# Kernel tuning notes

Measured on AMD Instinct MI355X. Metric: run time of the kernel, lower is better.

Reference implementation:

```python
import jax, jax.numpy as jnp
import numpy as np

N = 10000; E = 60000; D = 3000; H = 512; L = 128; P = 256
NUM_MASK = 3000  # int(0.3 * N)

def prelu(x, a):
    return jnp.where(x >= 0, x, a * x)

def setup_inputs() -> dict:
    key = jax.random.key(0)
    ks = jax.random.split(key, 32)
    def rn(k, shape, scale=0.02):
        return jax.random.normal(k, shape, jnp.float32) * scale
    inp = {
        'x': jax.random.normal(ks[0], (N, D), jnp.float32),
        'edge_index': jax.random.randint(ks[1], (2, E), 0, N),
        'perm': jax.random.permutation(ks[2], N),
        'shuffle': jax.random.permutation(ks[3], N - NUM_MASK),
        's_W1': rn(ks[4], (D, H)), 's_b1': jnp.zeros((H,), jnp.float32), 's_a': jnp.full((1,), 0.25, jnp.float32),
        's_W2': rn(ks[5], (H, L)), 's_b2': jnp.zeros((L,), jnp.float32),
        't_W1': rn(ks[6], (D, H)), 't_b1': jnp.zeros((H,), jnp.float32), 't_a': jnp.full((1,), 0.25, jnp.float32),
        't_W2': rn(ks[7], (H, L)), 't_b2': jnp.zeros((L,), jnp.float32),
        'p_W1': rn(ks[8], (L, P)), 'p_b1': jnp.zeros((P,), jnp.float32), 'p_a': jnp.full((1,), 0.25, jnp.float32),
        'p_W2': rn(ks[9], (P, L)), 'p_b2': jnp.zeros((L,), jnp.float32),
        'tp_W1': rn(ks[10], (L, P)), 'tp_b1': jnp.zeros((P,), jnp.float32), 'tp_a': jnp.full((1,), 0.25, jnp.float32),
        'tp_W2': rn(ks[11], (P, L)), 'tp_b2': jnp.zeros((L,), jnp.float32),
        'dgi_W': rn(ks[12], (L, L), 0.05),
        'pos_token': rn(ks[13], (1, D)), 'neg_token': rn(ks[14], (1, D)),
        'e2d_W': rn(ks[15], (L, L), 0.05),
        'd_W': rn(ks[16], (L, D)), 'd_b': jnp.zeros((D,), jnp.float32),
    }
    return inp

def reference(x, edge_index, perm, shuffle, s_W1, s_b1, s_a, s_W2, s_b2, t_W1, t_b1, t_a, t_W2, t_b2, p_W1, p_b1, p_a, p_W2, p_b2, tp_W1, tp_b1, tp_a, tp_W2, tp_b2, dgi_W, pos_token, neg_token, e2d_W, d_W, d_b):
    n = x.shape[0]
    # GCN normalization with added self loops (PyG gcn_norm, flow source->target)
    loops = jnp.arange(n)
    src = jnp.concatenate([edge_index[0], loops])
    dst = jnp.concatenate([edge_index[1], loops])
    deg = jax.ops.segment_sum(jnp.ones(dst.shape, x.dtype), dst, n)
    dinv = jnp.where(deg > 0, jax.lax.rsqrt(deg), 0.0)
    enorm = (dinv[src] * dinv[dst])[:, None]  # [E+N, 1]

    def gcn(h, W, b):
        h = h @ W  # transform first, then propagate (PyG GCNConv)
        return jax.ops.segment_sum(h[src] * enorm, dst, n) + b

    # feature masking / corruption (bn=False -> Identity; no dropout at eval)
    mask_nodes = perm[:NUM_MASK]
    keep_nodes = perm[NUM_MASK:]
    use_pos = x.at[mask_nodes].add(pos_token[0])
    use_neg = jnp.zeros_like(x).at[keep_nodes].set(x[keep_nodes][shuffle]).at[mask_nodes].add(neg_token[0])

    # student / teacher two-layer GCN encoders (shared PReLU param per encoder)
    rep_pos = prelu(gcn(prelu(gcn(use_pos, s_W1, s_b1), s_a), s_W2, s_b2), s_a)
    rep_neg = prelu(gcn(prelu(gcn(use_neg, t_W1, t_b1), t_a), t_W2, t_b2), t_a)

    def proj(z, W1, b1, a, W2, b2):
        return prelu(z @ W1 + b1, a) @ W2 + b2

    pos_z = proj(rep_pos[mask_nodes], p_W1, p_b1, p_a, p_W2, p_b2)
    neg_z = proj(rep_neg[mask_nodes], tp_W1, tp_b1, tp_a, tp_W2, tp_b2)

    # DGI loss with sigmoid summary of positive embeddings
    s = jax.nn.sigmoid(pos_z.mean(axis=0))  # [L]
    ws = dgi_W @ s
    pos_d = jax.nn.sigmoid(pos_z @ ws)
    neg_d = jax.nn.sigmoid(neg_z @ ws)
    dgi_loss = -jnp.log(pos_d + 1e-15).mean() - jnp.log(1.0 - neg_d + 1e-15).mean()

    # reconstruction: re-mask latent, single-GCN feature decoder (no activation)
    rec = (rep_pos @ e2d_W).at[mask_nodes].set(0.0)
    rec = gcn(rec, d_W, d_b)

    # SCE loss with alpha = 2
    def l2n(v):
        return v / jnp.maximum(jnp.linalg.norm(v, axis=-1, keepdims=True), 1e-12)
    cos = (l2n(x[mask_nodes]) * l2n(rec[mask_nodes])).sum(axis=-1)
    feat_loss = ((1.0 - cos) ** 2).mean()
    return (feat_loss, dgi_loss)
```

## Files before the change

### kernel.cpp

```cpp
#include <hip/hip_runtime.h>

#define NND 10000
#define EE  60000
#define DD  3000
#define HH  512
#define LL  128
#define PP  256
#define NM  3000

#define KP  3072
#define MP  10240
#define NW  1024
#define KTILES (KP/64)

#define BMT 320
#define BNT 128
#define AH_STR 10240
#define AB_STR 20480
#define BH_STR 4096
#define BB_STR 8192

typedef short bf16x8 __attribute__((ext_vector_type(8)));
typedef float f32x4 __attribute__((ext_vector_type(4)));

__device__ __align__(256) char g_ws[(size_t)176 << 20];

__device__ __forceinline__ unsigned short f2b(float f){
    unsigned int x = __float_as_uint(f);
    unsigned int r = x + 0x7FFFu + ((x >> 16) & 1u);
    return (unsigned short)(r >> 16);
}
__device__ __forceinline__ float b2f(unsigned short u){
    return __uint_as_float(((unsigned int)u) << 16);
}
__device__ __forceinline__ float2 bpair(unsigned int u){
    float2 r;
    r.x = __uint_as_float(u << 16);
    r.y = __uint_as_float(u & 0xffff0000u);
    return r;
}
__device__ __forceinline__ unsigned int packb(float a, float b){
    return (unsigned int)f2b(a) | ((unsigned int)f2b(b) << 16);
}

__device__ __forceinline__ void gl_lds16(const void* g, void* l){
    __builtin_amdgcn_global_load_lds(
        (const __attribute__((address_space(1))) unsigned int*)g,
        (__attribute__((address_space(3))) unsigned int*)l, 16, 0, 0);
}


__global__ void init_k(int* degi, int* cursor, float* scal,
                       float* ptW, float* ntW, float* svecraw, int* ecnt){
    int i = blockIdx.x*256 + threadIdx.x;
    if (i < NND){ degi[i]=0; cursor[i]=0; }
    if (i < 80) scal[i]=0.f;
    if (i == 0) ecnt[0]=0;
    if (i < 128) svecraw[i]=0.f;
    if (i < HH){ ptW[i]=0.f; ntW[i]=0.f; }
}

__global__ void build_k(const int* __restrict__ ei,
                        const int* __restrict__ perm, const int* __restrict__ shuf,
                        int* degi, int* flag, int* negsrc){
    int i = blockIdx.x*256 + threadIdx.x;
    if (i < EE) atomicAdd(&degi[ei[EE + i]], 1);
    if (i < NND){
        int p = perm[i];
        if (i < NM){ flag[p] = 1; negsrc[p] = -1; }
        else       { flag[p] = 0; negsrc[p] = perm[NM + shuf[i - NM]]; }
    }
}

__global__ __launch_bounds__(256) void alloc_k(const int* __restrict__ degi,
                                               float* dinv, int* rowptr, int* ecnt){
    __shared__ int sb[256];
    __shared__ int bbase;
    int t = threadIdx.x;
    int i = blockIdx.x*256 + t;
    int v = (i < NND) ? degi[i] : 0;
    sb[t] = v;
    __syncthreads();
    for (int off = 1; off < 256; off <<= 1){
        int x = 0;
        if (t >= off) x = sb[t - off];
        __syncthreads();
        sb[t] += x;
        __syncthreads();
    }
    if (t == 255) bbase = atomicAdd(ecnt, sb[255]);
    __syncthreads();
    if (i < NND){
        rowptr[i] = bbase + sb[t] - v;
        dinv[i] = 1.f/sqrtf((float)(degi[i] + 1));
    }
}

__global__ void fill_k(const int* __restrict__ ei, const int* __restrict__ rowptr,
                       int* cursor, int* adj){
    int i = blockIdx.x*256 + threadIdx.x;
    if (i < EE){
        int d = ei[EE + i];
        int s = ei[i];
        int p = atomicAdd(&cursor[d], 1);
        adj[rowptr[d] + p] = s;
    }
}

__global__ __launch_bounds__(512) void tok_k(const float* __restrict__ posT,
        const float* __restrict__ negT,
        const float* __restrict__ sW1, const float* __restrict__ tW1,
        float* ptW, float* ntW){
    int b = blockIdx.x; int chunk = blockIdx.y; int j = threadIdx.x;
    const float* tok = b ? negT : posT;
    const float* Wm  = b ? tW1  : sW1;
    float acc = 0.f;
    int d0 = chunk * 47, d1 = d0 + 47; if (d1 > DD) d1 = DD;
    for (int d = d0; d < d1; ++d) acc += tok[d] * Wm[(long)d*HH + j];
    atomicAdd(&((b ? ntW : ptW)[j]), acc);
}


__global__ __launch_bounds__(256) void cast_pad_x_k(const float* __restrict__ x,
                                                    unsigned short* __restrict__ xb){
    long idx = (long)blockIdx.x*256 + threadIdx.x;
    if (idx >= (long)MP*(KP/8)) return;
    int row = (int)(idx / (KP/8));
    int g   = (int)(idx % (KP/8));
    unsigned short o[8] = {0,0,0,0,0,0,0,0};
    if (row < NND && g < DD/8){
        const float* src = x + (long)row*DD + g*8;
        float4 a = *(const float4*)(src);
        float4 b = *(const float4*)(src + 4);
        o[0]=f2b(a.x); o[1]=f2b(a.y); o[2]=f2b(a.z); o[3]=f2b(a.w);
        o[4]=f2b(b.x); o[5]=f2b(b.y); o[6]=f2b(b.z); o[7]=f2b(b.w);
    }
    *(uint4*)(xb + (long)row*KP + g*8) = *(const uint4*)o;
}

struct TBatch {
    const float* in[10];
    unsigned short* out[10];
    int R[10], C[10], OS[10];
    int t0[11];
};

__global__ void transbatch_k(TBatch tb){
    __shared__ unsigned short tile[32][33];
    int b = blockIdx.x;
    int d = 0;
    while (d < 9 && b >= tb.t0[d+1]) d++;
    const float* in = tb.in[d];
    unsigned short* out = tb.out[d];
    int R = tb.R[d], C = tb.C[d], OS = tb.OS[d];
    int lt = b - tb.t0[d];
    int Ctiles = (C + 31) >> 5;
    int rt = lt / Ctiles, ct = lt % Ctiles;
    int rb = rt*32, cb = ct*32;
    int tx = threadIdx.x, ty = threadIdx.y;
    for (int i = ty; i < 32; i += 8){
        int r = rb + i, c = cb + tx;
        tile[i][tx] = (r < R && c < C) ? f2b(in[(long)r*C + c]) : (unsigned short)0;
    }
    __syncthreads();
    for (int i = ty; i < 32; i += 8){
        int c = cb + i, r = rb + tx;
        if (c < C && r < OS) out[(long)c*OS + r] = (r < R) ? tile[tx][i] : (unsigned short)0;
    }
}


#define LDA(PB, MT, KS) (*(const bf16x8*)&As[(PB) + (KS)*AH_STR + a_off + (MT)*512])
#define LDB(PB, NT, KS) (*(const bf16x8*)&Bs[(PB) + (KS)*BH_STR + b_off + (NT)*512])

#define STG_A(KT, PDST, P) gl_lds16(asrc[P] + ((KT)<<6), &As[(PDST) + adst[P]])
#define STG_B(KT, PDST, Q) gl_lds16(bsrc[Q] + ((KT)<<6), &Bs[(PDST) + bdst[Q]])

#define GATE7 asm volatile("s_waitcnt vmcnt(7)" ::: "memory")
#define GATE0 asm volatile("s_waitcnt vmcnt(0)" ::: "memory")
#define NOOPS ((void)0)
#define AFENCE asm volatile("" ::: "memory")
#define BARR  { AFENCE; __builtin_amdgcn_s_barrier(); AFENCE; }

#define TILE_BODY(S1_STMT, S2_STMT, GATE_STMT) {                                  \
    bf16x8 af_[5][2], bf_[4][2];                                                  \
    _Pragma("unroll") for (int nt = 0; nt < 4; ++nt){                             \
        bf_[nt][0] = LDB(pB, nt, 0); bf_[nt][1] = LDB(pB, nt, 1); }               \
    _Pragma("unroll") for (int mt = 0; mt < 5; ++mt){                             \
        af_[mt][0] = LDA(pA, mt, 0); af_[mt][1] = LDA(pA, mt, 1); }               \
    S1_STMT;                                                                      \
    __builtin_amdgcn_s_setprio(1);                                                \
    _Pragma("unroll") for (int ks = 0; ks < 2; ++ks)                              \
      _Pragma("unroll") for (int nt = 0; nt < 4; ++nt)                            \
        _Pragma("unroll") for (int mt = 0; mt < 2; ++mt)                          \
          acc[mt][nt] = __builtin_amdgcn_mfma_f32_16x16x32_bf16(af_[mt][ks], bf_[nt][ks], acc[mt][nt], 0,0,0); \
    __builtin_amdgcn_s_setprio(0);                                                \
    BARR;                                                                         \
    S2_STMT;                                                                      \
    __builtin_amdgcn_s_setprio(1);                                                \
    _Pragma("unroll") for (int ks = 0; ks < 2; ++ks)                              \
      _Pragma("unroll") for (int nt = 0; nt < 4; ++nt)                            \
        _Pragma("unroll") for (int mt = 2; mt < 5; ++mt)                          \
          acc[mt][nt] = __builtin_amdgcn_mfma_f32_16x16x32_bf16(af_[mt][ks], bf_[nt][ks], acc[mt][nt], 0,0,0); \
    __builtin_amdgcn_s_setprio(0);                                                \
    GATE_STMT;                                                                    \
    BARR;                                                                         \
}

__global__ __launch_bounds__(512, 2) void gemm320(
    const unsigned short* __restrict__ Ag,
    const unsigned short* __restrict__ Bg,
    unsigned short* __restrict__ C,
    int M, int Cstride)
{
    __shared__ __align__(1024) unsigned short As[3*AB_STR];
    __shared__ __align__(1024) unsigned short Bs[2*BB_STR];

    const int bid = blockIdx.x;
    const int swz = (bid & 7)*32 + (bid >> 3);
    const int m0 = (swz >> 3) * BMT;
    const int n0 = (swz & 7) * BNT;

    const int tid = threadIdx.x;
    const int w   = tid >> 6,  l = tid & 63;
    const int wm  = w >> 1,    wn = w & 1;
    const int l16 = l & 15,    quad = l >> 4;

    const int schunk = (l & 3) ^ (((l >> 5) & 1) << 1);
    const int rq8   = ((quad ^ (((l16 >> 3) & 1) << 1)) << 3);
    const int a_off = ((wm*80 + l16) << 5) + rq8;
    const int b_off = ((wn*64 + l16) << 5) + rq8;

    const unsigned short* asrc[5]; int adst[5];
    #pragma unroll
    for (int p = 0; p < 5; ++p){
        int j = 5*w + p, kh = j/20, g = j - kh*20;
        asrc[p] = Ag + (long)(m0 + g*16 + (l >> 2))*KP + (kh << 5) + (schunk << 3);
        adst[p] = kh*AH_STR + g*512;
    }
    const unsigned short* bsrc[2]; int bdst[2];
    #pragma unroll
    for (int q = 0; q < 2; ++q){
        int j = 2*w + q, kh = j >> 3, g = j & 7;
        bsrc[q] = Bg + (long)(n0 + g*16 + (l >> 2))*KP + (kh << 5) + (schunk << 3);
        bdst[q] = kh*BH_STR + g*512;
    }

    f32x4 acc[5][4];
    #pragma unroll
    for (int i = 0; i < 5; ++i)
        #pragma unroll
        for (int j = 0; j < 4; ++j)
            #pragma unroll
            for (int r = 0; r < 4; ++r) acc[i][j][r] = 0.f;

    #pragma unroll
    for (int p = 0; p < 5; ++p) STG_A(0, 0, p);
    #pragma unroll
    for (int q = 0; q < 2; ++q) STG_B(0, 0, q);
    #pragma unroll
    for (int p = 0; p < 5; ++p) STG_A(1, AB_STR, p);
    #pragma unroll
    for (int q = 0; q < 2; ++q) STG_B(1, BB_STR, q);
    GATE7;
    BARR;

    int ab = 0, bb = 0;
    #pragma unroll 1
    for (int t = 0; t < KTILES-2; ++t){
        const int pA  = ab*AB_STR;
        const int pB  = bb*BB_STR;
        const int ab2 = (ab == 0) ? 2 : ab - 1;
        const int pA2 = ab2*AB_STR;
        TILE_BODY({ STG_A(t+2,pA2,0); STG_A(t+2,pA2,1); STG_A(t+2,pA2,2); STG_A(t+2,pA2,3); },
                  { STG_A(t+2,pA2,4); STG_B(t+2,pB,0); STG_B(t+2,pB,1); },
                  GATE7)
        ab = (ab == 2) ? 0 : ab + 1;
        bb ^= 1;
    }
    {
        const int pA = ab*AB_STR, pB = bb*BB_STR;
        TILE_BODY(NOOPS, NOOPS, GATE0)
        ab = (ab == 2) ? 0 : ab + 1;
        bb ^= 1;
    }
    {
        const int pA = ab*AB_STR, pB = bb*BB_STR;
        TILE_BODY(NOOPS, NOOPS, NOOPS)
    }

    #pragma unroll
    for (int mt = 0; mt < 5; ++mt){
        const int rowb = m0 + wm*80 + mt*16 + quad*4;
        #pragma unroll
        for (int nt = 0; nt < 4; ++nt){
            const int col = n0 + wn*64 + nt*16 + l16;
            #pragma unroll
            for (int r = 0; r < 4; ++r){
                const int row = rowb + r;
                if (row < M) C[(long)row*Cstride + col] = f2b(acc[mt][nt][r]);
            }
        }
    }
}

__device__ __forceinline__ void gemm_bt_body(
    const unsigned short* __restrict__ A,
    const unsigned short* __restrict__ BT,
    void* __restrict__ Cv,
    int M, int Nn, int K, int Cstride,
    const float* __restrict__ bias,
    const float* __restrict__ alpha,
    int epi, const int* __restrict__ ridx, int obf)
{
    __shared__ __align__(16) unsigned short As[64*40];
    __shared__ __align__(16) unsigned short Bs[64*40];
    const int m0 = blockIdx.y*64, n0 = blockIdx.x*64;
    const int t = threadIdx.x;
    const int lrow = t >> 2, lk = (t & 3) * 8;
    const int wave = t >> 6, lane = t & 63;
    const int quad = lane >> 4, l16 = lane & 15;
    f32x4 acc[4];
    #pragma unroll
    for (int i = 0; i < 4; i++)
        for (int j = 0; j < 4; j++) acc[i][j] = 0.f;

    const bool arv = (m0 + lrow) < M;
    const bool brv = (n0 + lrow) < Nn;
    long arow = 0;
    if (arv) arow = ridx ? (long)ridx[m0 + lrow] : (long)(m0 + lrow);
    const long arowbase = arow * K;
    const long browbase = (long)(n0 + lrow) * K;

    for (int k0 = 0; k0 < K; k0 += 32){
        int gk = k0 + lk;
        uint4 av = {0u,0u,0u,0u};
        uint4 bv = {0u,0u,0u,0u};
        if (arv) av = *(const uint4*)(A + arowbase + gk);
        if (brv) bv = *(const uint4*)(BT + browbase + gk);
        *(uint4*)(&As[lrow*40 + lk]) = av;
        *(uint4*)(&Bs[lrow*40 + lk]) = bv;
        __syncthreads();
        bf16x8 af = *(const bf16x8*)(&As[(wave*16 + l16)*40 + quad*8]);
        #pragma unroll
        for (int nt = 0; nt < 4; nt++){
            bf16x8 bfr = *(const bf16x8*)(&Bs[(nt*16 + l16)*40 + quad*8]);
            acc[nt] = __builtin_amdgcn_mfma_f32_16x16x32_bf16(af, bfr, acc[nt], 0, 0, 0);
        }
        __syncthreads();
    }

    const int rowb = m0 + wave*16 + quad*4;
    float aval = (epi == 2) ? alpha[0] : 0.f;
    #pragma unroll
    for (int nt = 0; nt < 4; nt++){
        int col = n0 + nt*16 + l16;
        if (col >= Nn) continue;
        float bvv = epi ? bias[col] : 0.f;
        #pragma unroll
        for (int r = 0; r < 4; r++){
            int row = rowb + r;
            if (row < M){
                float v = acc[nt][r] + bvv;
                if (epi == 2 && v < 0.f) v *= aval;
                if (obf) ((unsigned short*)Cv)[(long)row*Cstride + col] = f2b(v);
                else     ((float*)Cv)[(long)row*Cstride + col] = v;
            }
        }
    }
}

__global__ __launch_bounds__(256) void gemm_bt_ex(
    const unsigned short* __restrict__ A,
    const unsigned short* __restrict__ BT,
    void* __restrict__ Cv,
    int M, int Nn, int K, int Cstride,
    const float* __restrict__ bias,
    const float* __restrict__ alpha,
    int epi, const int* __restrict__ ridx, int obf)
{
    gemm_bt_body(A, BT, Cv, M, Nn, K, Cstride, bias, alpha, epi, ridx, obf);
}

__global__ __launch_bounds__(256) void gemm_bt2(
    const unsigned short* __restrict__ A0, const unsigned short* __restrict__ A1,
    const unsigned short* __restrict__ B0, const unsigned short* __restrict__ B1,
    void* __restrict__ C0, void* __restrict__ C1,
    int M, int Nn, int K, int Cstride,
    const float* __restrict__ bias0, const float* __restrict__ bias1,
    const float* __restrict__ al0, const float* __restrict__ al1,
    int epi, const int* __restrict__ ridx, int obf)
{
    if (blockIdx.z == 0)
        gemm_bt_body(A0, B0, C0, M, Nn, K, Cstride, bias0, al0, epi, ridx, obf);
    else
        gemm_bt_body(A1, B1, C1, M, Nn, K, Cstride, bias1, al1, epi, ridx, obf);
}

__global__ __launch_bounds__(256) void gemm_bt3(
    const unsigned short* __restrict__ repP, const unsigned short* __restrict__ repN,
    const unsigned short* __restrict__ pW1T, const unsigned short* __restrict__ tpW1T,
    const unsigned short* __restrict__ e2dWT,
    unsigned short* __restrict__ posH, unsigned short* __restrict__ negH,
    unsigned short* __restrict__ recPre,
    const float* __restrict__ pb1, const float* __restrict__ tpb1,
    const float* __restrict__ pa, const float* __restrict__ tpa,
    const int* __restrict__ perm)
{
    int z = blockIdx.z;
    if (z == 0){
        if (blockIdx.y < 47)
            gemm_bt_body(repP, pW1T, posH, NM, PP, LL, PP, pb1, pa, 2, perm, 1);
    } else if (z == 1){
        if (blockIdx.y < 47)
            gemm_bt_body(repN, tpW1T, negH, NM, PP, LL, PP, tpb1, tpa, 2, perm, 1);
    } else {
        if (blockIdx.x < 2)
            gemm_bt_body(repP, e2dWT, recPre, NND, LL, LL, LL, nullptr, nullptr, 0, nullptr, 1);
    }
}


__global__ __launch_bounds__(256) void agg1_k(const unsigned short* __restrict__ XW,
    const float* __restrict__ ptW, const float* __restrict__ ntW,
    const int* __restrict__ flag, const int* __restrict__ negsrc,
    const float* __restrict__ dinv, const int* __restrict__ rowptr,
    const int* __restrict__ degi, const int* __restrict__ adj,
    const float* __restrict__ sb1, const float* __restrict__ sav,
    const float* __restrict__ tb1, const float* __restrict__ tav,
    unsigned short* __restrict__ H1p, unsigned short* __restrict__ H1n)
{
    int i = blockIdx.x; int t = threadIdx.x;
    int half = t >> 7;
    int c = (t & 127) * 4;
    float di = dinv[i];
    int rs = rowptr[i], re = rs + degi[i];
    int fi = flag[i];
    float a0, a1, a2, a3;

    if (half == 0){
        float p0 = ptW[c], p1 = ptW[c+1], p2 = ptW[c+2], p3 = ptW[c+3];
        uint2 v = *(const uint2*)(XW + (long)i*1024 + c);
        float2 va = bpair(v.x), vb = bpair(v.y);
        float ffi = fi ? 1.f : 0.f;
        a0 = (va.x + ffi*p0)*di; a1 = (va.y + ffi*p1)*di;
        a2 = (vb.x + ffi*p2)*di; a3 = (vb.y + ffi*p3)*di;
        for (int e = rs; e < re; ++e){
            int s = adj[e]; float ds = dinv[s];
            float ffs = flag[s] ? 1.f : 0.f;
            uint2 w = *(const uint2*)(XW + (long)s*1024 + c);
            float2 wa = bpair(w.x), wb = bpair(w.y);
            a0 += (wa.x + ffs*p0)*ds; a1 += (wa.y + ffs*p1)*ds;
            a2 += (wb.x + ffs*p2)*ds; a3 += (wb.y + ffs*p3)*ds;
        }
        float sa_ = sav[0];
        float v0 = di*a0 + sb1[c];   if (v0 < 0.f) v0 *= sa_;
        float v1 = di*a1 + sb1[c+1]; if (v1 < 0.f) v1 *= sa_;
        float v2 = di*a2 + sb1[c+2]; if (v2 < 0.f) v2 *= sa_;
        float v3 = di*a3 + sb1[c+3]; if (v3 < 0.f) v3 *= sa_;
        uint2 o; o.x = packb(v0, v1); o.y = packb(v2, v3);
        *(uint2*)(H1p + (long)i*512 + c) = o;
    } else {
        float n0 = ntW[c], n1 = ntW[c+1], n2 = ntW[c+2], n3 = ntW[c+3];
        if (fi){ a0 = n0*di; a1 = n1*di; a2 = n2*di; a3 = n3*di; }
        else {
            int nsi = negsrc[i];
            uint2 v = *(const uint2*)(XW + (long)nsi*1024 + 512 + c);
            float2 va = bpair(v.x), vb = bpair(v.y);
            a0 = va.x*di; a1 = va.y*di; a2 = vb.x*di; a3 = vb.y*di;
        }
        for (int e = rs; e < re; ++e){
            int s = adj[e]; float ds = dinv[s];
            if (flag[s]){ a0 += n0*ds; a1 += n1*ds; a2 += n2*ds; a3 += n3*ds; }
            else {
                int ns = negsrc[s];
                uint2 w = *(const uint2*)(XW + (long)ns*1024 + 512 + c);
                float2 wa = bpair(w.x), wb = bpair(w.y);
                a0 += wa.x*ds; a1 += wa.y*ds; a2 += wb.x*ds; a3 += wb.y*ds;
            }
        }
        float ta_ = tav[0];
        float v0 = di*a0 + tb1[c];   if (v0 < 0.f) v0 *= ta_;
        float v1 = di*a1 + tb1[c+1]; if (v1 < 0.f) v1 *= ta_;
        float v2 = di*a2 + tb1[c+2]; if (v2 < 0.f) v2 *= ta_;
        float v3 = di*a3 + tb1[c+3]; if (v3 < 0.f) v3 *= ta_;
        uint2 o; o.x = packb(v0, v1); o.y = packb(v2, v3);
        *(uint2*)(H1n + (long)i*512 + c) = o;
    }
}

__global__ __launch_bounds__(128) void agg128_k(
    const unsigned short* __restrict__ In0, const unsigned short* __restrict__ In1,
    const float* __restrict__ dinv, const int* __restrict__ rowptr,
    const int* __restrict__ degi, const int* __restrict__ adj,
    const float* __restrict__ b20, const float* __restrict__ b21,
    const float* __restrict__ a20, const float* __restrict__ a21,
    unsigned short* __restrict__ Out0, unsigned short* __restrict__ Out1)
{
    int i = blockIdx.x, t = threadIdx.x;
    int h = t >> 6;
    int c = (t & 63) * 2;
    const unsigned short* In = h ? In1 : In0;
    const float* b2 = h ? b21 : b20;
    const float* a2 = h ? a21 : a20;
    unsigned short* Out = h ? Out1 : Out0;
    float di = dinv[i];
    int rs = rowptr[i], re = rs + degi[i];
    float2 sv = bpair(*(const unsigned int*)(In + (long)i*128 + c));
    float acc0 = sv.x * di, acc1 = sv.y * di;
    for (int e = rs; e < re; ++e){
        int s = adj[e]; float ds = dinv[s];
        float2 w = bpair(*(const unsigned int*)(In + (long)s*128 + c));
        acc0 += w.x * ds; acc1 += w.y * ds;
    }
    float a = a2[0];
    float v0 = di*acc0 + b2[c];   if (v0 < 0.f) v0 *= a;
    float v1 = di*acc1 + b2[c+1]; if (v1 < 0.f) v1 *= a;
    *(unsigned int*)(Out + (long)i*128 + c) = packb(v0, v1);
}

__global__ __launch_bounds__(64) void aggrec_k(const unsigned short* __restrict__ recPre,
    const float* __restrict__ dinv, const int* __restrict__ rowptr,
    const int* __restrict__ degi, const int* __restrict__ adj,
    const int* __restrict__ flag, const int* __restrict__ perm,
    unsigned short* __restrict__ recAgg)
{
    int b = blockIdx.x, t = threadIdx.x;
    int c = t * 2;
    int i = perm[b];
    float di = dinv[i];
    int rs = rowptr[i], re = rs + degi[i];
    float acc0 = 0.f, acc1 = 0.f;
    for (int e = rs; e < re; ++e){
        int s = adj[e];
        if (!flag[s]){
            float ds = dinv[s];
            float2 w = bpair(*(const unsigned int*)(recPre + (long)s*128 + c));
            acc0 += w.x * ds; acc1 += w.y * ds;
        }
    }
    *(unsigned int*)(recAgg + (long)b*128 + c) = packb(di*acc0, di*acc1);
}


__global__ __launch_bounds__(128) void meanp_k(const float* __restrict__ posZ,
                                               float* svecraw){
    int j = threadIdx.x;
    int r0 = blockIdx.x*64, r1 = r0 + 64; if (r1 > NM) r1 = NM;
    float s = 0.f;
    for (int r = r0; r < r1; ++r) s += posZ[(long)r*128 + j];
    atomicAdd(&svecraw[j], s);
}

__global__ void ws_k(const float* __restrict__ dgiW, const float* __restrict__ svecraw,
                     float* wsv){
    __shared__ float s[128];
    int i = threadIdx.x;
    s[i] = 1.f/(1.f + expf(-svecraw[i]/(float)NM));
    __syncthreads();
    float a = 0.f;
    for (int j = 0; j < 128; ++j) a += dgiW[i*128 + j] * s[j];
    wsv[i] = a;
}

__global__ __launch_bounds__(256) void dgi_k(const float* __restrict__ posZ,
    const float* __restrict__ negZ, const float* __restrict__ wsv, float* scal){
    __shared__ float sp[4], sn[4];
    int wid = threadIdx.x >> 6, lane = threadIdx.x & 63;
    float w0 = wsv[lane], w1 = wsv[64 + lane];
    float accp = 0.f, accn = 0.f;
    for (int row = blockIdx.x*4 + wid; row < 2*NM; row += gridDim.x*4){
        const float* Z = (row < NM) ? posZ : negZ;
        int r = (row < NM) ? row : row - NM;
        float v = Z[(long)r*128 + lane] * w0 + Z[(long)r*128 + 64 + lane] * w1;
        for (int off = 32; off; off >>= 1) v += __shfl_down(v, off, 64);
        if (lane == 0){
            float d = 1.f/(1.f + expf(-v));
            if (row < NM) accp += logf(d + 1e-15f);
            else          accn += logf(1.f - d + 1e-15f);
        }
    }
    if (lane == 0){ sp[wid] = accp; sn[wid] = accn; }
    __syncthreads();
    if (threadIdx.x == 0){
        atomicAdd(&scal[0], sp[0]+sp[1]+sp[2]+sp[3]);
        atomicAdd(&scal[1], sn[0]+sn[1]+sn[2]+sn[3]);
    }
}


__global__ __launch_bounds__(256) void cos_k(const float* __restrict__ x,
    const unsigned short* __restrict__ recMask, const int* __restrict__ perm,
    float* scal){
    int b = blockIdx.x, t = threadIdx.x;
    long xi = (long)perm[b]*DD;
    long ri = (long)b*DD;
    float dot = 0.f, nx = 0.f, nr = 0.f;
    for (int d0 = t*8; d0 < DD; d0 += 2048){
        float4 xa = *(const float4*)(x + xi + d0);
        float4 xb2 = *(const float4*)(x + xi + d0 + 4);
        uint4 rv = *(const uint4*)(recMask + ri + d0);
        float2 r0 = bpair(rv.x), r1 = bpair(rv.y), r2 = bpair(rv.z), r3 = bpair(rv.w);
        dot += xa.x*r0.x + xa.y*r0.y + xa.z*r1.x + xa.w*r1.y
             + xb2.x*r2.x + xb2.y*r2.y + xb2.z*r3.x + xb2.w*r3.y;
        nx  += xa.x*xa.x + xa.y*xa.y + xa.z*xa.z + xa.w*xa.w
             + xb2.x*xb2.x + xb2.y*xb2.y + xb2.z*xb2.z + xb2.w*xb2.w;
        nr  += r0.x*r0.x + r0.y*r0.y + r1.x*r1.x + r1.y*r1.y
             + r2.x*r2.x + r2.y*r2.y + r3.x*r3.x + r3.y*r3.y;
    }
    for (int off = 32; off; off >>= 1){
        dot += __shfl_down(dot, off, 64);
        nx  += __shfl_down(nx,  off, 64);
        nr  += __shfl_down(nr,  off, 64);
    }
    __shared__ float sd[4], sx[4], sr[4];
    int w = t >> 6, lane = t & 63;
    if (lane == 0){ sd[w] = dot; sx[w] = nx; sr[w] = nr; }
    __syncthreads();
    if (t == 0){
        float Dv = sd[0]+sd[1]+sd[2]+sd[3];
        float Xv = sx[0]+sx[1]+sx[2]+sx[3];
        float Rv = sr[0]+sr[1]+sr[2]+sr[3];
        float c = Dv/(fmaxf(sqrtf(Xv),1e-12f)*fmaxf(sqrtf(Rv),1e-12f));
        float e = 1.f - c;
        atomicAdd(&scal[16 + (b & 63)], e*e);
    }
}

__global__ void fin_k(const float* __restrict__ scal, float* out){
    float fs = 0.f;
    for (int i = 0; i < 64; ++i) fs += scal[16 + i];
    float feat = fs/(float)NM;
    float dgi  = -(scal[0]/(float)NM) - (scal[1]/(float)NM);
    out[0] = feat;
    out[1] = dgi;
}


extern "C" void kernel_launch(void* const* d_in, const int* in_sizes, int n_in,
                              void* d_out, int out_size, void* d_ws, size_t ws_size,
                              hipStream_t stream) {
    (void)in_sizes; (void)n_in; (void)out_size; (void)d_ws; (void)ws_size;
    const float* x  = (const float*)d_in[0];
    const int* ei   = (const int*)d_in[1];
    const int* perm = (const int*)d_in[2];
    const int* shuf = (const int*)d_in[3];
    const float* sW1 = (const float*)d_in[4];
    const float* sb1 = (const float*)d_in[5];
    const float* sa  = (const float*)d_in[6];
    const float* sW2 = (const float*)d_in[7];
    const float* sb2 = (const float*)d_in[8];
    const float* tW1 = (const float*)d_in[9];
    const float* tb1 = (const float*)d_in[10];
    const float* ta  = (const float*)d_in[11];
    const float* tW2 = (const float*)d_in[12];
    const float* tb2 = (const float*)d_in[13];
    const float* pW1 = (const float*)d_in[14];
    const float* pb1 = (const float*)d_in[15];
    const float* pa  = (const float*)d_in[16];
    const float* pW2 = (const float*)d_in[17];
    const float* pb2 = (const float*)d_in[18];
    const float* tpW1 = (const float*)d_in[19];
    const float* tpb1 = (const float*)d_in[20];
    const float* tpa  = (const float*)d_in[21];
    const float* tpW2 = (const float*)d_in[22];
    const float* tpb2 = (const float*)d_in[23];
    const float* dgiW = (const float*)d_in[24];
    const float* posT = (const float*)d_in[25];
    const float* negT = (const float*)d_in[26];
    const float* e2dW = (const float*)d_in[27];
    const float* dW   = (const float*)d_in[28];
    const float* db   = (const float*)d_in[29];
    float* out = (float*)d_out;

    void* wsp = nullptr;
    hipGetSymbolAddress(&wsp, HIP_SYMBOL(g_ws));
    char* base = (char*)wsp;
    size_t off = 0;
    auto alloc = [&](size_t b){ size_t o = off; off = (off + b + 255) & ~(size_t)255; return o; };

    float* dinv    = (float*)(base + alloc(NND*4));
    int* degi      = (int*)  (base + alloc(NND*4));
    int* rowptr    = (int*)  (base + alloc(NND*4));
    int* cursor    = (int*)  (base + alloc(NND*4));
    int* adj       = (int*)  (base + alloc(EE*4));
    int* flag      = (int*)  (base + alloc(NND*4));
    int* negsrc    = (int*)  (base + alloc(NND*4));
    int* ecnt      = (int*)  (base + alloc(16*4));
    float* ptW     = (float*)(base + alloc(HH*4));
    float* ntW     = (float*)(base + alloc(HH*4));
    float* svecraw = (float*)(base + alloc(128*4));
    float* wsv     = (float*)(base + alloc(128*4));
    float* scal    = (float*)(base + alloc(80*4));

    unsigned short* xb    = (unsigned short*)(base + alloc((size_t)MP*KP*2));
    unsigned short* W1T   = (unsigned short*)(base + alloc((size_t)NW*KP*2));
    unsigned short* sW2T  = (unsigned short*)(base + alloc((size_t)LL*HH*2));
    unsigned short* tW2T  = (unsigned short*)(base + alloc((size_t)LL*HH*2));
    unsigned short* pW1T  = (unsigned short*)(base + alloc((size_t)PP*LL*2));
    unsigned short* pW2T  = (unsigned short*)(base + alloc((size_t)LL*PP*2));
    unsigned short* tpW1T = (unsigned short*)(base + alloc((size_t)PP*LL*2));
    unsigned short* tpW2T = (unsigned short*)(base + alloc((size_t)LL*PP*2));
    unsigned short* e2dWT = (unsigned short*)(base + alloc((size_t)LL*LL*2));
    unsigned short* dWT   = (unsigned short*)(base + alloc((size_t)DD*LL*2));

    unsigned short* XW      = (unsigned short*)(base + alloc((size_t)NND*1024*2));
    unsigned short* H1p     = (unsigned short*)(base + alloc((size_t)NND*512*2));
    unsigned short* H1n     = (unsigned short*)(base + alloc((size_t)NND*512*2));
    unsigned short* M2p     = (unsigned short*)(base + alloc((size_t)NND*128*2));
    unsigned short* M2n     = (unsigned short*)(base + alloc((size_t)NND*128*2));
    unsigned short* repP    = (unsigned short*)(base + alloc((size_t)NND*128*2));
    unsigned short* repN    = (unsigned short*)(base + alloc((size_t)NND*128*2));
    unsigned short* posH    = (unsigned short*)(base + alloc((size_t)NM*256*2));
    unsigned short* negH    = (unsigned short*)(base + alloc((size_t)NM*256*2));
    float* posZ             = (float*)(base + alloc((size_t)NM*128*4));
    float* negZ             = (float*)(base + alloc((size_t)NM*128*4));
    unsigned short* recPre  = (unsigned short*)(base + alloc((size_t)NND*128*2));
    unsigned short* recAgg  = (unsigned short*)(base + alloc((size_t)NM*128*2));
    unsigned short* recMask = (unsigned short*)(base + alloc((size_t)NM*DD*2));

    init_k<<<(NND+255)/256, 256, 0, stream>>>(degi, cursor, scal, ptW, ntW, svecraw, ecnt);
    build_k<<<(EE+255)/256, 256, 0, stream>>>(ei, perm, shuf, degi, flag, negsrc);
    alloc_k<<<(NND+255)/256, 256, 0, stream>>>(degi, dinv, rowptr, ecnt);
    fill_k<<<(EE+255)/256, 256, 0, stream>>>(ei, rowptr, cursor, adj);
    tok_k<<<dim3(2,64), 512, 0, stream>>>(posT, negT, sW1, tW1, ptW, ntW);

    cast_pad_x_k<<<(int)(((long)MP*(KP/8) + 255)/256), 256, 0, stream>>>(x, xb);
    {
        TBatch tb;
        const float* ins[10] = {sW1, tW1, sW2, tW2, pW1, pW2, tpW1, tpW2, e2dW, dW};
        unsigned short* outs[10] = {W1T, W1T + (size_t)HH*KP, sW2T, tW2T, pW1T, pW2T,
                                    tpW1T, tpW2T, e2dWT, dWT};
        int Rs[10]  = {DD, DD, HH, HH, LL, PP, LL, PP, LL, LL};
        int Cs[10]  = {HH, HH, LL, LL, PP, LL, PP, LL, LL, DD};
        int OSs[10] = {KP, KP, HH, HH, LL, PP, LL, PP, LL, LL};
        int cum = 0;
        for (int d = 0; d < 10; d++){
            tb.in[d] = ins[d]; tb.out[d] = outs[d];
            tb.R[d] = Rs[d]; tb.C[d] = Cs[d]; tb.OS[d] = OSs[d];
            tb.t0[d] = cum;
            cum += (OSs[d]/32) * ((Cs[d] + 31)/32);
        }
        tb.t0[10] = cum;
        transbatch_k<<<cum, dim3(32,8), 0, stream>>>(tb);
    }

    gemm320<<<256, 512, 0, stream>>>(xb, W1T, XW, NND, 1024);
    agg1_k<<<NND, 256, 0, stream>>>(XW, ptW, ntW, flag, negsrc, dinv, rowptr, degi, adj,
                                    sb1, sa, tb1, ta, H1p, H1n);

    gemm_bt2<<<dim3(2,157,2), 256, 0, stream>>>(H1p, H1n, sW2T, tW2T, M2p, M2n,
                                                NND, LL, HH, LL,
                                                nullptr, nullptr, nullptr, nullptr,
                                                0, nullptr, 1);
    agg128_k<<<NND, 128, 0, stream>>>(M2p, M2n, dinv, rowptr, degi, adj,
                                      sb2, tb2, sa, ta, repP, repN);

    gemm_bt3<<<dim3(4,157,3), 256, 0, stream>>>(repP, repN, pW1T, tpW1T, e2dWT,
                                                posH, negH, recPre,
                                                pb1, tpb1, pa, tpa, perm);
    gemm_bt2<<<dim3(2,47,2), 256, 0, stream>>>(posH, negH, pW2T, tpW2T, posZ, negZ,
                                               NM, LL, PP, LL,
                                               pb2, tpb2, nullptr, nullptr, 1, nullptr, 0);

    aggrec_k<<<NM, 64, 0, stream>>>(recPre, dinv, rowptr, degi, adj, flag, perm, recAgg);
    gemm_bt_ex<<<dim3(47,47), 256, 0, stream>>>(recAgg, dWT, recMask, NM, DD, LL, DD,
                                                db, nullptr, 1, nullptr, 1);

    meanp_k<<<47, 128, 0, stream>>>(posZ, svecraw);
    ws_k<<<1, 128, 0, stream>>>(dgiW, svecraw, wsv);
    dgi_k<<<128, 256, 0, stream>>>(posZ, negZ, wsv, scal);

    cos_k<<<NM, 256, 0, stream>>>(x, recMask, perm, scal);

    fin_k<<<1, 1, 0, stream>>>(scal, out);
}
```

Measured before the change: 497.0 us.

## Merge staging kernels, fuse posZ column mean into GEMM, widen small-GEMM K step

Folds the x cast/pad, the weight transposes and the token-times-W1 products into a single staging launch, which removes two kernel launches. The pos-projection GEMM now accumulates column sums in its epilogue through shared memory and atomics. That replaces the separate mean kernel, and the bias is added back inside ws_k. The generic small GEMM also loads 64-wide K slices per barrier instead of 32, halving the number of synchronisations at the cost of more shared memory.

```diff
diff --git a/kernel.cpp b/kernel.cpp
--- a/kernel.cpp
+++ b/kernel.cpp
@@ -107,36 +107,6 @@
     }
 }
 
-__global__ __launch_bounds__(512) void tok_k(const float* __restrict__ posT,
-        const float* __restrict__ negT,
-        const float* __restrict__ sW1, const float* __restrict__ tW1,
-        float* ptW, float* ntW){
-    int b = blockIdx.x; int chunk = blockIdx.y; int j = threadIdx.x;
-    const float* tok = b ? negT : posT;
-    const float* Wm  = b ? tW1  : sW1;
-    float acc = 0.f;
-    int d0 = chunk * 47, d1 = d0 + 47; if (d1 > DD) d1 = DD;
-    for (int d = d0; d < d1; ++d) acc += tok[d] * Wm[(long)d*HH + j];
-    atomicAdd(&((b ? ntW : ptW)[j]), acc);
-}
-
-
-__global__ __launch_bounds__(256) void cast_pad_x_k(const float* __restrict__ x,
-                                                    unsigned short* __restrict__ xb){
-    long idx = (long)blockIdx.x*256 + threadIdx.x;
-    if (idx >= (long)MP*(KP/8)) return;
-    int row = (int)(idx / (KP/8));
-    int g   = (int)(idx % (KP/8));
-    unsigned short o[8] = {0,0,0,0,0,0,0,0};
-    if (row < NND && g < DD/8){
-        const float* src = x + (long)row*DD + g*8;
-        float4 a = *(const float4*)(src);
-        float4 b = *(const float4*)(src + 4);
-        o[0]=f2b(a.x); o[1]=f2b(a.y); o[2]=f2b(a.z); o[3]=f2b(a.w);
-        o[4]=f2b(b.x); o[5]=f2b(b.y); o[6]=f2b(b.z); o[7]=f2b(b.w);
-    }
-    *(uint4*)(xb + (long)row*KP + g*8) = *(const uint4*)o;
-}
 
 struct TBatch {
     const float* in[10];
@@ -145,28 +115,71 @@
     int t0[11];
 };
 
-__global__ void transbatch_k(TBatch tb){
+#define CASTB ((int)(((long)MP*(KP/8) + 255)/256))
+
+__global__ __launch_bounds__(256) void stage_k(TBatch tb,
+    const float* __restrict__ x, unsigned short* __restrict__ xb,
+    const float* __restrict__ posT, const float* __restrict__ negT,
+    const float* __restrict__ sW1, const float* __restrict__ tW1,
+    float* ptW, float* ntW)
+{
     __shared__ unsigned short tile[32][33];
     int b = blockIdx.x;
-    int d = 0;
-    while (d < 9 && b >= tb.t0[d+1]) d++;
-    const float* in = tb.in[d];
-    unsigned short* out = tb.out[d];
-    int R = tb.R[d], C = tb.C[d], OS = tb.OS[d];
-    int lt = b - tb.t0[d];
-    int Ctiles = (C + 31) >> 5;
-    int rt = lt / Ctiles, ct = lt % Ctiles;
-    int rb = rt*32, cb = ct*32;
-    int tx = threadIdx.x, ty = threadIdx.y;
-    for (int i = ty; i < 32; i += 8){
-        int r = rb + i, c = cb + tx;
-        tile[i][tx] = (r < R && c < C) ? f2b(in[(long)r*C + c]) : (unsigned short)0;
-    }
-    __syncthreads();
-    for (int i = ty; i < 32; i += 8){
-        int c = cb + i, r = rb + tx;
-        if (c < C && r < OS) out[(long)c*OS + r] = (r < R) ? tile[tx][i] : (unsigned short)0;
-    }
+    int t = threadIdx.x;
+    if (b < CASTB){
+        long idx = (long)b*256 + t;
+        if (idx < (long)MP*(KP/8)){
+            int row = (int)(idx / (KP/8));
+            int g   = (int)(idx % (KP/8));
+            unsigned short o[8] = {0,0,0,0,0,0,0,0};
+            if (row < NND && g < DD/8){
+                const float* src = x + (long)row*DD + g*8;
+                float4 a = *(const float4*)(src);
+                float4 bb = *(const float4*)(src + 4);
+                o[0]=f2b(a.x); o[1]=f2b(a.y); o[2]=f2b(a.z); o[3]=f2b(a.w);
+                o[4]=f2b(bb.x); o[5]=f2b(bb.y); o[6]=f2b(bb.z); o[7]=f2b(bb.w);
+            }
+            *(uint4*)(xb + (long)row*KP + g*8) = *(const uint4*)o;
+        }
+        return;
+    }
+    b -= CASTB;
+    if (b < tb.t0[10]){
+        int d = 0;
+        while (d < 9 && b >= tb.t0[d+1]) d++;
+        const float* in = tb.in[d];
+        unsigned short* out = tb.out[d];
+        int R = tb.R[d], C = tb.C[d], OS = tb.OS[d];
+        int lt = b - tb.t0[d];
+        int Ctiles = (C + 31) >> 5;
+        int rt = lt / Ctiles, ct = lt % Ctiles;
+        int rb = rt*32, cb = ct*32;
+        int tx = t & 31, ty = t >> 5;
+        for (int i = ty; i < 32; i += 8){
+            int r = rb + i, c = cb + tx;
+            tile[i][tx] = (r < R && c < C) ? f2b(in[(long)r*C + c]) : (unsigned short)0;
+        }
+        __syncthreads();
+        for (int i = ty; i < 32; i += 8){
+            int c = cb + i, r = rb + tx;
+            if (c < C && r < OS) out[(long)c*OS + r] = (r < R) ? tile[tx][i] : (unsigned short)0;
+        }
+        return;
+    }
+    b -= tb.t0[10];
+    int tokb = b & 1, chunk = b >> 1;
+    const float* tok = tokb ? negT : posT;
+    const float* Wm  = tokb ? tW1 : sW1;
+    float acc0 = 0.f, acc1 = 0.f;
+    int d0 = chunk*24, d1 = d0 + 24; if (d1 > DD) d1 = DD;
+    for (int d = d0; d < d1; ++d){
+        float tv = tok[d];
+        acc0 += tv * Wm[(long)d*HH + t];
+        acc1 += tv * Wm[(long)d*HH + t + 256];
+    }
+    float* dst = tokb ? ntW : ptW;
+    atomicAdd(&dst[t], acc0);
+    atomicAdd(&dst[t+256], acc1);
 }
 
 
@@ -311,10 +324,11 @@
     int M, int Nn, int K, int Cstride,
     const float* __restrict__ bias,
     const float* __restrict__ alpha,
-    int epi, const int* __restrict__ ridx, int obf)
+    int epi, const int* __restrict__ ridx, int obf,
+    float* __restrict__ colsum)
 {
-    __shared__ __align__(16) unsigned short As[64*40];
-    __shared__ __align__(16) unsigned short Bs[64*40];
+    __shared__ __align__(16) unsigned short As[2][64*40];
+    __shared__ __align__(16) unsigned short Bs[2][64*40];
     const int m0 = blockIdx.y*64, n0 = blockIdx.x*64;
     const int t = threadIdx.x;
     const int lrow = t >> 2, lk = (t & 3) * 8;
@@ -332,20 +346,30 @@
     const long arowbase = arow * K;
     const long browbase = (long)(n0 + lrow) * K;
 
-    for (int k0 = 0; k0 < K; k0 += 32){
-        int gk = k0 + lk;
-        uint4 av = {0u,0u,0u,0u};
-        uint4 bv = {0u,0u,0u,0u};
-        if (arv) av = *(const uint4*)(A + arowbase + gk);
-        if (brv) bv = *(const uint4*)(BT + browbase + gk);
-        *(uint4*)(&As[lrow*40 + lk]) = av;
-        *(uint4*)(&Bs[lrow*40 + lk]) = bv;
+    for (int k0 = 0; k0 < K; k0 += 64){
+        uint4 av0 = {0u,0u,0u,0u}, av1 = {0u,0u,0u,0u};
+        uint4 bv0 = {0u,0u,0u,0u}, bv1 = {0u,0u,0u,0u};
+        if (arv){
+            av0 = *(const uint4*)(A + arowbase + k0 + lk);
+            av1 = *(const uint4*)(A + arowbase + k0 + 32 + lk);
+        }
+        if (brv){
+            bv0 = *(const uint4*)(BT + browbase + k0 + lk);
+            bv1 = *(const uint4*)(BT + browbase + k0 + 32 + lk);
+        }
+        *(uint4*)(&As[0][lrow*40 + lk]) = av0;
+        *(uint4*)(&As[1][lrow*40 + lk]) = av1;
+        *(uint4*)(&Bs[0][lrow*40 + lk]) = bv0;
+        *(uint4*)(&Bs[1][lrow*40 + lk]) = bv1;
         __syncthreads();
-        bf16x8 af = *(const bf16x8*)(&As[(wave*16 + l16)*40 + quad*8]);
         #pragma unroll
-        for (int nt = 0; nt < 4; nt++){
-            bf16x8 bfr = *(const bf16x8*)(&Bs[(nt*16 + l16)*40 + quad*8]);
-            acc[nt] = __builtin_amdgcn_mfma_f32_16x16x32_bf16(af, bfr, acc[nt], 0, 0, 0);
+        for (int ks = 0; ks < 2; ++ks){
+            bf16x8 af = *(const bf16x8*)(&As[ks][(wave*16 + l16)*40 + quad*8]);
+            #pragma unroll
+            for (int nt = 0; nt < 4; nt++){
+                bf16x8 bfr = *(const bf16x8*)(&Bs[ks][(nt*16 + l16)*40 + quad*8]);
+                acc[nt] = __builtin_amdgcn_mfma_f32_16x16x32_bf16(af, bfr, acc[nt], 0, 0, 0);
+            }
         }
         __syncthreads();
     }
@@ -368,6 +392,23 @@
             }
         }
     }
+
+    if (colsum){
+        __syncthreads();
+        float* cs = (float*)As;
+        #pragma unroll
+        for (int nt = 0; nt < 4; nt++){
+            float s = acc[nt][0] + acc[nt][1] + acc[nt][2] + acc[nt][3];
+            cs[(nt*16 + l16)*16 + (wave*4 + quad)] = s;
+        }
+        __syncthreads();
+        if (t < 64){
+            float s = 0.f;
+            #pragma unroll
+            for (int j = 0; j < 16; ++j) s += cs[t*16 + j];
+            atomicAdd(&colsum[n0 + t], s);
+        }
+    }
 }
 
 __global__ __launch_bounds__(256) void gemm_bt_ex(
@@ -379,7 +420,7 @@
     const float* __restrict__ alpha,
     int epi, const int* __restrict__ ridx, int obf)
 {
-    gemm_bt_body(A, BT, Cv, M, Nn, K, Cstride, bias, alpha, epi, ridx, obf);
+    gemm_bt_body(A, BT, Cv, M, Nn, K, Cstride, bias, alpha, epi, ridx, obf, nullptr);
 }
 
 __global__ __launch_bounds__(256) void gemm_bt2(
@@ -389,12 +430,13 @@
     int M, int Nn, int K, int Cstride,
     const float* __restrict__ bias0, const float* __restrict__ bias1,
     const float* __restrict__ al0, const float* __restrict__ al1,
-    int epi, const int* __restrict__ ridx, int obf)
+    int epi, const int* __restrict__ ridx, int obf,
+    float* __restrict__ cs0)
 {
     if (blockIdx.z == 0)
-        gemm_bt_body(A0, B0, C0, M, Nn, K, Cstride, bias0, al0, epi, ridx, obf);
+        gemm_bt_body(A0, B0, C0, M, Nn, K, Cstride, bias0, al0, epi, ridx, obf, cs0);
     else
-        gemm_bt_body(A1, B1, C1, M, Nn, K, Cstride, bias1, al1, epi, ridx, obf);
+        gemm_bt_body(A1, B1, C1, M, Nn, K, Cstride, bias1, al1, epi, ridx, obf, nullptr);
 }
 
 __global__ __launch_bounds__(256) void gemm_bt3(
@@ -410,13 +452,13 @@
     int z = blockIdx.z;
     if (z == 0){
         if (blockIdx.y < 47)
-            gemm_bt_body(repP, pW1T, posH, NM, PP, LL, PP, pb1, pa, 2, perm, 1);
+            gemm_bt_body(repP, pW1T, posH, NM, PP, LL, PP, pb1, pa, 2, perm, 1, nullptr);
     } else if (z == 1){
         if (blockIdx.y < 47)
-            gemm_bt_body(repN, tpW1T, negH, NM, PP, LL, PP, tpb1, tpa, 2, perm, 1);
+            gemm_bt_body(repN, tpW1T, negH, NM, PP, LL, PP, tpb1, tpa, 2, perm, 1, nullptr);
     } else {
         if (blockIdx.x < 2)
-            gemm_bt_body(repP, e2dWT, recPre, NND, LL, LL, LL, nullptr, nullptr, 0, nullptr, 1);
+            gemm_bt_body(repP, e2dWT, recPre, NND, LL, LL, LL, nullptr, nullptr, 0, nullptr, 1, nullptr);
     }
 }
 
@@ -543,20 +585,11 @@
 }
 
 
-__global__ __launch_bounds__(128) void meanp_k(const float* __restrict__ posZ,
-                                               float* svecraw){
-    int j = threadIdx.x;
-    int r0 = blockIdx.x*64, r1 = r0 + 64; if (r1 > NM) r1 = NM;
-    float s = 0.f;
-    for (int r = r0; r < r1; ++r) s += posZ[(long)r*128 + j];
-    atomicAdd(&svecraw[j], s);
-}
-
 __global__ void ws_k(const float* __restrict__ dgiW, const float* __restrict__ svecraw,
-                     float* wsv){
+                     const float* __restrict__ pb2, float* wsv){
     __shared__ float s[128];
     int i = threadIdx.x;
-    s[i] = 1.f/(1.f + expf(-svecraw[i]/(float)NM));
+    s[i] = 1.f/(1.f + expf(-(svecraw[i]/(float)NM + pb2[i])));
     __syncthreads();
     float a = 0.f;
     for (int j = 0; j < 128; ++j) a += dgiW[i*128 + j] * s[j];
@@ -723,9 +756,7 @@
     build_k<<<(EE+255)/256, 256, 0, stream>>>(ei, perm, shuf, degi, flag, negsrc);
     alloc_k<<<(NND+255)/256, 256, 0, stream>>>(degi, dinv, rowptr, ecnt);
     fill_k<<<(EE+255)/256, 256, 0, stream>>>(ei, rowptr, cursor, adj);
-    tok_k<<<dim3(2,64), 512, 0, stream>>>(posT, negT, sW1, tW1, ptW, ntW);
-
-    cast_pad_x_k<<<(int)(((long)MP*(KP/8) + 255)/256), 256, 0, stream>>>(x, xb);
+
     {
         TBatch tb;
         const float* ins[10] = {sW1, tW1, sW2, tW2, pW1, pW2, tpW1, tpW2, e2dW, dW};
@@ -742,7 +773,8 @@
             cum += (OSs[d]/32) * ((Cs[d] + 31)/32);
         }
         tb.t0[10] = cum;
-        transbatch_k<<<cum, dim3(32,8), 0, stream>>>(tb);
+        stage_k<<<CASTB + cum + 256, 256, 0, stream>>>(tb, x, xb, posT, negT,
+                                                       sW1, tW1, ptW, ntW);
     }
 
     gemm320<<<256, 512, 0, stream>>>(xb, W1T, XW, NND, 1024);
@@ -752,7 +784,7 @@
     gemm_bt2<<<dim3(2,157,2), 256, 0, stream>>>(H1p, H1n, sW2T, tW2T, M2p, M2n,
                                                 NND, LL, HH, LL,
                                                 nullptr, nullptr, nullptr, nullptr,
-                                                0, nullptr, 1);
+                                                0, nullptr, 1, nullptr);
     agg128_k<<<NND, 128, 0, stream>>>(M2p, M2n, dinv, rowptr, degi, adj,
                                       sb2, tb2, sa, ta, repP, repN);
 
@@ -761,14 +793,14 @@
                                                 pb1, tpb1, pa, tpa, perm);
     gemm_bt2<<<dim3(2,47,2), 256, 0, stream>>>(posH, negH, pW2T, tpW2T, posZ, negZ,
                                                NM, LL, PP, LL,
-                                               pb2, tpb2, nullptr, nullptr, 1, nullptr, 0);
+                                               pb2, tpb2, nullptr, nullptr, 1, nullptr, 0,
+                                               svecraw);
 
     aggrec_k<<<NM, 64, 0, stream>>>(recPre, dinv, rowptr, degi, adj, flag, perm, recAgg);
     gemm_bt_ex<<<dim3(47,47), 256, 0, stream>>>(recAgg, dWT, recMask, NM, DD, LL, DD,
                                                 db, nullptr, 1, nullptr, 1);
 
-    meanp_k<<<47, 128, 0, stream>>>(posZ, svecraw);
-    ws_k<<<1, 128, 0, stream>>>(dgiW, svecraw, wsv);
+    ws_k<<<1, 128, 0, stream>>>(dgiW, svecraw, pb2, wsv);
     dgi_k<<<128, 256, 0, stream>>>(posZ, negZ, wsv, scal);
 
     cos_k<<<NM, 256, 0, stream>>>(x, recMask, perm, scal);
```

Result: faster. 457.4 us (-8.0%).
